# Performance work log

Hardware: AMD Instinct MI355X
Metric: run time of the kernel (lower is better)

Reference implementation:

```python
import jax, jax.numpy as jnp
import numpy as np

EMBED = 1024
HEADS = 16
HEAD_DIM = EMBED // HEADS
HIDDEN = 4096
EPS = 1e-5


def setup_inputs() -> dict:
    key = jax.random.key(0)
    ks = jax.random.split(key, 12)
    s_e = 1.0 / np.sqrt(EMBED)
    s_h = 1.0 / np.sqrt(HIDDEN)
    inp = {
        'x': jax.random.normal(ks[0], (2, 2048, EMBED), jnp.float32),
        'Wq': jax.random.uniform(ks[1], (EMBED, EMBED), jnp.float32, -s_e, s_e),
        'bq': jnp.zeros((EMBED,), jnp.float32),
        'Wk': jax.random.uniform(ks[2], (EMBED, EMBED), jnp.float32, -s_e, s_e),
        'bk': jnp.zeros((EMBED,), jnp.float32),
        'Wv': jax.random.uniform(ks[3], (EMBED, EMBED), jnp.float32, -s_e, s_e),
        'bv': jnp.zeros((EMBED,), jnp.float32),
        'Wo': jax.random.uniform(ks[4], (EMBED, EMBED), jnp.float32, -s_e, s_e),
        'bo': jnp.zeros((EMBED,), jnp.float32),
        'g1': jnp.ones((EMBED,), jnp.float32),
        'b1': jnp.zeros((EMBED,), jnp.float32),
        'W1': jax.random.uniform(ks[5], (EMBED, HIDDEN), jnp.float32, -s_e, s_e),
        'bm1': jnp.zeros((HIDDEN,), jnp.float32),
        'W2': jax.random.uniform(ks[6], (HIDDEN, EMBED), jnp.float32, -s_h, s_h),
        'bm2': jnp.zeros((EMBED,), jnp.float32),
        'g2': jnp.ones((EMBED,), jnp.float32),
        'b2': jnp.zeros((EMBED,), jnp.float32),
    }
    return inp


def _layernorm(x, g, b):
    mu = jnp.mean(x, axis=-1, keepdims=True)
    var = jnp.mean(jnp.square(x - mu), axis=-1, keepdims=True)
    return (x - mu) * jax.lax.rsqrt(var + EPS) * g + b


def _attention(x, Wq, bq, Wk, bk, Wv, bv, Wo, bo):
    b, n, d = x.shape
    def split(h):  # [b,n,d] -> [b,H,n,hd]
        return h.reshape(b, n, HEADS, HEAD_DIM).transpose(0, 2, 1, 3)
    q = split(x @ Wq + bq)
    k = split(x @ Wk + bk)
    v = split(x @ Wv + bv)
    # NOTE: original multiplies by sqrt(head_dim) (bug preserved for faithfulness)
    scores = jnp.einsum('bhqd,bhkd->bhqk', q, k) * jnp.sqrt(jnp.float32(HEAD_DIM))
    causal = jnp.tril(jnp.ones((n, n), bool))
    scores = jnp.where(causal, scores, -jnp.inf)
    attn = jax.nn.softmax(scores, axis=-1)
    out = jnp.einsum('bhqk,bhkd->bhqd', attn, v)
    out = out.transpose(0, 2, 1, 3).reshape(b, n, d)
    return out @ Wo + bo


def reference(x, Wq, bq, Wk, bk, Wv, bv, Wo, bo, g1, b1, W1, bm1, W2, bm2, g2, b2):
    res1 = x
    x = _layernorm(_attention(x, Wq, bq, Wk, bk, Wv, bv, Wo, bo), g1, b1) + res1
    res2 = x
    h = jax.nn.gelu(x @ W1 + bm1, approximate=False) @ W2 + bm2
    return _layernorm(h, g2, b2) + res2
```

## Files before the change

kernel.cpp:

```cpp
#include <hip/hip_runtime.h>
#include <stdint.h>

typedef unsigned short u16;
typedef short short8 __attribute__((ext_vector_type(8)));
typedef float f32x4 __attribute__((ext_vector_type(4)));
typedef u16 u16x4 __attribute__((ext_vector_type(4)));
typedef u16 u16x8 __attribute__((ext_vector_type(8)));

#define MODE_F32  0
#define MODE_GELU 2
#define MODE_VT   4

__device__ __forceinline__ float b2f(u16 v) {
    union { uint32_t u; float f; } x; x.u = ((uint32_t)v) << 16; return x.f;
}
__device__ __forceinline__ u16 f2b(float f) {
    union { float f; uint32_t u; } x; x.f = f;
    uint32_t u = x.u;
    return (u16)((u + 0x7FFFu + ((u >> 16) & 1u)) >> 16);
}

#define ASYNC16(gp, lp)                                                        \
    __builtin_amdgcn_global_load_lds(                                          \
        (const __attribute__((address_space(1))) uint32_t*)(const void*)(gp),  \
        (__attribute__((address_space(3))) uint32_t*)(void*)(lp), 16, 0, 0)

#define MFMA16(a, b, c) __builtin_amdgcn_mfma_f32_16x16x32_bf16((a), (b), (c), 0, 0, 0)

__global__ __launch_bounds__(256) void split_f32(
    const float* __restrict__ in, u16* __restrict__ hi, u16* __restrict__ lo)
{
    const int i = (blockIdx.x * 256 + threadIdx.x) * 4;
    f32x4 v = *(const f32x4*)&in[i];
    u16x4 h, l;
    for (int k = 0; k < 4; k++) {
        h[k] = f2b(v[k]);
        l[k] = f2b(v[k] - b2f(h[k]));
    }
    *(u16x4*)&hi[i] = h;
    *(u16x4*)&lo[i] = l;
}

__global__ __launch_bounds__(256) void transpose_f32_bf16(
    const float* __restrict__ in, u16* __restrict__ out, int rows, int cols)
{
    __shared__ float t[32][33];
    const int r0 = blockIdx.y * 32, c0 = blockIdx.x * 32;
    const int tr = threadIdx.x >> 3, tc = (threadIdx.x & 7) * 4;
    f32x4 v = *(const f32x4*)&in[(size_t)(r0 + tr) * cols + c0 + tc];
    for (int i = 0; i < 4; i++) t[tr][tc + i] = v[i];
    __syncthreads();
    u16x4 ov;
    for (int i = 0; i < 4; i++) ov[i] = f2b(t[tc + i][tr]);
    *(u16x4*)&out[(size_t)(c0 + tr) * rows + r0 + tc] = ov;
}

__global__ __launch_bounds__(256) void transpose_split_f32(
    const float* __restrict__ in, u16* __restrict__ hi, u16* __restrict__ lo,
    int rows, int cols)
{
    __shared__ float t[32][33];
    const int r0 = blockIdx.y * 32, c0 = blockIdx.x * 32;
    const int tr = threadIdx.x >> 3, tc = (threadIdx.x & 7) * 4;
    f32x4 v = *(const f32x4*)&in[(size_t)(r0 + tr) * cols + c0 + tc];
    for (int i = 0; i < 4; i++) t[tr][tc + i] = v[i];
    __syncthreads();
    u16x4 hv, lv;
    for (int i = 0; i < 4; i++) {
        const float f = t[tc + i][tr];
        hv[i] = f2b(f);
        lv[i] = f2b(f - b2f(hv[i]));
    }
    const size_t o = (size_t)(c0 + tr) * rows + r0 + tc;
    *(u16x4*)&hi[o] = hv;
    *(u16x4*)&lo[o] = lv;
}

__global__ __launch_bounds__(256) void gemm_qk_x3(
    const u16* __restrict__ Ahi, const u16* __restrict__ Alo,
    const u16* __restrict__ Bhi, const u16* __restrict__ Blo,
    const float* __restrict__ bq, const float* __restrict__ bk,
    u16* __restrict__ Qhi, u16* __restrict__ Qlo,
    u16* __restrict__ Khi, u16* __restrict__ Klo)
{
    const int K = 1024;
    __shared__ __align__(16) u16 SM[32768];
    u16* lAh = SM;          u16* lAl = SM + 8192;
    u16* lBh = SM + 16384;  u16* lBl = SM + 24576;

    const int tid = threadIdx.x;
    const int w = tid >> 6, lane = tid & 63;
    const int lane15 = lane & 15, q = lane >> 4;
    const int tM = blockIdx.y * 128, tN = blockIdx.x * 128;
    const int m0 = (w >> 1) * 64, n0 = (w & 1) * 64;

    f32x4 acc[4][4];
    for (int i = 0; i < 4; i++)
        for (int j = 0; j < 4; j++)
            acc[i][j] = (f32x4){0.f, 0.f, 0.f, 0.f};

    const int pa0 = 2 * w, pa1 = 2 * w + 1;
    const int srow = lane >> 2, sch = lane & 3;
    const u16* Ah = Ahi + (size_t)tM * K;
    const u16* Al = Alo + (size_t)tM * K;
    const u16* Bh = Bhi + (size_t)tN * K;
    const u16* Bl = Blo + (size_t)tN * K;
    const size_t r0 = (size_t)(pa0 * 16 + srow) * K + sch * 8;
    const size_t r1 = (size_t)(pa1 * 16 + srow) * K + sch * 8;

    ASYNC16(Ah + r0, lAh + pa0 * 512);  ASYNC16(Ah + r1, lAh + pa1 * 512);
    ASYNC16(Al + r0, lAl + pa0 * 512);  ASYNC16(Al + r1, lAl + pa1 * 512);
    ASYNC16(Bh + r0, lBh + pa0 * 512);  ASYNC16(Bh + r1, lBh + pa1 * 512);
    ASYNC16(Bl + r0, lBl + pa0 * 512);  ASYNC16(Bl + r1, lBl + pa1 * 512);

    const int NT = K / 32;
    for (int kt = 0; kt < NT; kt++) {
        __syncthreads();
        const int cb = (kt & 1) * 4096, nb = 4096 - cb;
        if (kt + 1 < NT) {
            const int k0 = (kt + 1) * 32;
            ASYNC16(Ah + r0 + k0, lAh + nb + pa0 * 512);  ASYNC16(Ah + r1 + k0, lAh + nb + pa1 * 512);
            ASYNC16(Al + r0 + k0, lAl + nb + pa0 * 512);  ASYNC16(Al + r1 + k0, lAl + nb + pa1 * 512);
            ASYNC16(Bh + r0 + k0, lBh + nb + pa0 * 512);  ASYNC16(Bh + r1 + k0, lBh + nb + pa1 * 512);
            ASYNC16(Bl + r0 + k0, lBl + nb + pa0 * 512);  ASYNC16(Bl + r1 + k0, lBl + nb + pa1 * 512);
        }
        short8 afh[4], afl[4], bfh[4], bfl[4];
        for (int i = 0; i < 4; i++) {
            const int o = cb + (m0 + i * 16 + lane15) * 32 + q * 8;
            afh[i] = *(const short8*)&lAh[o];
            afl[i] = *(const short8*)&lAl[o];
        }
        for (int j = 0; j < 4; j++) {
            const int o = cb + (n0 + j * 16 + lane15) * 32 + q * 8;
            bfh[j] = *(const short8*)&lBh[o];
            bfl[j] = *(const short8*)&lBl[o];
        }
        for (int i = 0; i < 4; i++)
            for (int j = 0; j < 4; j++) {
                acc[i][j] = MFMA16(afh[i], bfh[j], acc[i][j]);
                acc[i][j] = MFMA16(afh[i], bfl[j], acc[i][j]);
                acc[i][j] = MFMA16(afl[i], bfh[j], acc[i][j]);
            }
    }

    const bool isQ = (tN < 1024);
    u16* dhi = isQ ? Qhi : Khi;
    u16* dlo = isQ ? Qlo : Klo;
    const int cN = isQ ? tN : (tN - 1024);
    u16* sC = SM;
    for (int pass = 0; pass < 2; pass++) {
        __syncthreads();
        for (int i = 0; i < 4; i++) {
            const int rl0 = m0 + i * 16 + q * 4;
            for (int j = 0; j < 4; j++) {
                const int cl = n0 + j * 16 + lane15;
                const float bv = isQ ? bq[cN + cl] : bk[cN + cl];
                for (int r = 0; r < 4; r++) {
                    const float v = acc[i][j][r] + bv;
                    const u16 hv = f2b(v);
                    sC[(rl0 + r) * 136 + cl] = pass == 0 ? hv : f2b(v - b2f(hv));
                }
            }
        }
        __syncthreads();
        u16* dst = pass == 0 ? dhi : dlo;
        for (int t8 = 0; t8 < 8; t8++) {
            const int rl = t8 * 16 + (tid >> 4), cl = (tid & 15) * 8;
            *(u16x8*)&dst[(size_t)(tM + rl) * 1024 + cN + cl] = *(const u16x8*)&sC[rl * 136 + cl];
        }
    }
}

__global__ __launch_bounds__(256) void gemm_bt(
    const u16* __restrict__ A, const u16* __restrict__ Bt, const float* __restrict__ bias,
    int M, int N, int K, int mode,
    float* __restrict__ outF, u16* __restrict__ outB, size_t pstride)
{
    __shared__ __align__(16) u16 SM[17408];
    u16* lA = SM;
    u16* lB = SM + 8192;

    const int tid = threadIdx.x;
    const int w = tid >> 6, lane = tid & 63;
    const int lane15 = lane & 15, q = lane >> 4;
    const int tM = blockIdx.y * 128, tN = blockIdx.x * 128;
    const int m0 = (w >> 1) * 64, n0 = (w & 1) * 64;

    const int kchunk = K / gridDim.z;
    const int koff = blockIdx.z * kchunk;
    outF += (size_t)blockIdx.z * pstride;

    f32x4 acc[4][4];
    for (int i = 0; i < 4; i++)
        for (int j = 0; j < 4; j++)
            acc[i][j] = (f32x4){0.f, 0.f, 0.f, 0.f};

    const int pa0 = 2 * w, pa1 = 2 * w + 1;
    const int srow = lane >> 2, sch = lane & 3;
    const u16* Abase = A + (size_t)tM * K + koff;
    const u16* Bbase = Bt + (size_t)tN * K + koff;
    const size_t r0 = (size_t)(pa0 * 16 + srow) * K + sch * 8;
    const size_t r1 = (size_t)(pa1 * 16 + srow) * K + sch * 8;

    ASYNC16(Abase + r0, lA + pa0 * 512);
    ASYNC16(Abase + r1, lA + pa1 * 512);
    ASYNC16(Bbase + r0, lB + pa0 * 512);
    ASYNC16(Bbase + r1, lB + pa1 * 512);

    const int NT = kchunk / 32;
    for (int kt = 0; kt < NT; kt++) {
        __syncthreads();
        const int cb = (kt & 1) * 4096, nb = 4096 - cb;
        if (kt + 1 < NT) {
            const int k0 = (kt + 1) * 32;
            ASYNC16(Abase + r0 + k0, lA + nb + pa0 * 512);
            ASYNC16(Abase + r1 + k0, lA + nb + pa1 * 512);
            ASYNC16(Bbase + r0 + k0, lB + nb + pa0 * 512);
            ASYNC16(Bbase + r1 + k0, lB + nb + pa1 * 512);
        }
        short8 af[4], bf[4];
        for (int i = 0; i < 4; i++) af[i] = *(const short8*)&lA[cb + (m0 + i * 16 + lane15) * 32 + q * 8];
        for (int j = 0; j < 4; j++) bf[j] = *(const short8*)&lB[cb + (n0 + j * 16 + lane15) * 32 + q * 8];
        for (int i = 0; i < 4; i++)
            for (int j = 0; j < 4; j++)
                acc[i][j] = MFMA16(af[i], bf[j], acc[i][j]);
    }

    if (mode == MODE_F32) {
        for (int i = 0; i < 4; i++) {
            const int rb = tM + m0 + i * 16 + q * 4;
            for (int j = 0; j < 4; j++) {
                const int col = tN + n0 + j * 16 + lane15;
                const float bv = (bias && blockIdx.z == 0) ? bias[col] : 0.f;
                for (int r = 0; r < 4; r++)
                    outF[(size_t)(rb + r) * N + col] = acc[i][j][r] + bv;
            }
        }
        return;
    }

    u16* sC = SM;
    __syncthreads();
    if (mode == MODE_GELU) {
        for (int i = 0; i < 4; i++) {
            const int rl0 = m0 + i * 16 + q * 4;
            for (int j = 0; j < 4; j++) {
                const int cl = n0 + j * 16 + lane15;
                const float bv = bias[tN + cl];
                for (int r = 0; r < 4; r++) {
                    float v = acc[i][j][r] + bv;
                    v = 0.5f * v * (1.f + erff(v * 0.70710678118f));
                    sC[(rl0 + r) * 136 + cl] = f2b(v);
                }
            }
        }
        __syncthreads();
        for (int t8 = 0; t8 < 8; t8++) {
            const int rl = t8 * 16 + (tid >> 4), cl = (tid & 15) * 8;
            *(u16x8*)&outB[(size_t)(tM + rl) * N + tN + cl] = *(const u16x8*)&sC[rl * 136 + cl];
        }
    } else {
        for (int i = 0; i < 4; i++) {
            const int rl0 = m0 + i * 16 + q * 4;
            for (int j = 0; j < 4; j++) {
                const int cl = n0 + j * 16 + lane15;
                const float bv = bias[tN + cl];
                for (int r = 0; r < 4; r++)
                    sC[cl * 136 + rl0 + r] = f2b(acc[i][j][r] + bv);
            }
        }
        __syncthreads();
        const int bb = tM >> 11, nbase = tM & 2047;
        for (int t8 = 0; t8 < 8; t8++) {
            const int cl = t8 * 16 + (tid >> 4), rl = (tid & 15) * 8;
            const int colg = tN + cl;
            u16* dst = &outB[((size_t)(bb * 16 + (colg >> 6)) * 64 + (colg & 63)) * 2048 + nbase + rl];
            *(u16x8*)dst = *(const u16x8*)&sC[cl * 136 + rl];
        }
    }
}

__global__ __launch_bounds__(256) void attn_fwd(
    const u16* __restrict__ Qhig, const u16* __restrict__ Qlog,
    const u16* __restrict__ Khig, const u16* __restrict__ Klog,
    const u16* __restrict__ Vtg, u16* __restrict__ Og)
{
    __shared__ u16 lQh[2][2048], lQl[2][2048];
    __shared__ u16 lKh[2][1024], lKl[2][1024];
    __shared__ u16 lV[2048];
    __shared__ u16 lP[4][640];

    const int tid = threadIdx.x, w = tid >> 6, lane = tid & 63;
    const int lane15 = lane & 15, q = lane >> 4;
    const int bh = blockIdx.x >> 4, pair = blockIdx.x & 15;
    const int b = bh >> 4, h = bh & 15;

    const size_t xoff = (size_t)b * 2048 * 1024 + h * 64;
    const u16* Qh_ = Qhig + xoff;
    const u16* Ql_ = Qlog + xoff;
    const u16* Kh_ = Khig + xoff;
    const u16* Kl_ = Klog + xoff;
    const u16* Vbh = Vtg + (size_t)bh * 64 * 2048;
    u16* Obh = Og + xoff;

    const int srow = lane >> 2, sch = lane & 3;
    const float NEG = -3.0e38f;

    for (int half = 0; half < 2; half++) {
        const int qb = half ? (31 - pair) : pair;
        const int qrow0 = qb * 64;
        const int ntiles = 2 * qb + 2;

        for (int ii = 0; ii < 4; ii++) {
            const int id = w * 4 + ii;
            const int idq = id & 7, ks = idq >> 2, p = idq & 3;
            const size_t so = (size_t)(qrow0 + p * 16 + srow) * 1024 + ks * 32 + sch * 8;
            if (id < 8) ASYNC16(Qh_ + so, &lQh[ks][p * 512]);
            else        ASYNC16(Ql_ + so, &lQl[ks][p * 512]);
        }

        f32x4 o[4];
        for (int j = 0; j < 4; j++) o[j] = (f32x4){0.f, 0.f, 0.f, 0.f};
        float mrow[4], lrow[4];
        for (int r = 0; r < 4; r++) { mrow[r] = NEG; lrow[r] = 0.f; }
        short8 aqh0 = {}, aqh1 = {}, aql0 = {}, aql1 = {};
        bool first = true;

        for (int t = 0; t < ntiles; t++) {
            const int kk0 = t * 32;
            for (int ii = 0; ii < 3; ii++) {
                const int id = w * 3 + ii;
                if (id < 8) {
                    const int sel = id >> 2, idk = id & 3, ks = idk >> 1, hh = idk & 1;
                    const size_t so = (size_t)(kk0 + hh * 16 + srow) * 1024 + ks * 32 + sch * 8;
                    if (sel == 0) ASYNC16(Kh_ + so, &lKh[ks][hh * 512]);
                    else          ASYNC16(Kl_ + so, &lKl[ks][hh * 512]);
                } else {
                    const int p = id - 8;
                    ASYNC16(Vbh + (size_t)(p * 16 + srow) * 2048 + kk0 + sch * 8, &lV[p * 512]);
                }
            }
            __syncthreads();
            if (first) {
                const int o0 = (w * 16 + lane15) * 32 + q * 8;
                aqh0 = *(const short8*)&lQh[0][o0];
                aqh1 = *(const short8*)&lQh[1][o0];
                aql0 = *(const short8*)&lQl[0][o0];
                aql1 = *(const short8*)&lQl[1][o0];
                first = false;
            }
            f32x4 s[2];
            for (int sub = 0; sub < 2; sub++) {
                const int ko = (sub * 16 + lane15) * 32 + q * 8;
                short8 bkh0 = *(const short8*)&lKh[0][ko];
                short8 bkh1 = *(const short8*)&lKh[1][ko];
                short8 bkl0 = *(const short8*)&lKl[0][ko];
                short8 bkl1 = *(const short8*)&lKl[1][ko];
                f32x4 z = (f32x4){0.f, 0.f, 0.f, 0.f};
                z = MFMA16(aqh0, bkh0, z);
                z = MFMA16(aqh1, bkh1, z);
                z = MFMA16(aqh0, bkl0, z);
                z = MFMA16(aqh1, bkl1, z);
                z = MFMA16(aql0, bkh0, z);
                z = MFMA16(aql1, bkh1, z);
                s[sub] = z;
            }
            const int rbase = qrow0 + w * 16 + q * 4;
            for (int sub = 0; sub < 2; sub++)
                for (int r = 0; r < 4; r++) {
                    const int key = kk0 + sub * 16 + lane15;
                    float sv = s[sub][r] * 8.0f;
                    if (key > rbase + r) sv = NEG;
                    s[sub][r] = sv;
                }
            float mx[4];
            for (int r = 0; r < 4; r++) mx[r] = fmaxf(s[0][r], s[1][r]);
            for (int d = 1; d < 16; d <<= 1)
                for (int r = 0; r < 4; r++) mx[r] = fmaxf(mx[r], __shfl_xor(mx[r], d));
            float alpha[4];
            for (int r = 0; r < 4; r++) {
                const float mnew = fmaxf(mrow[r], mx[r]);
                alpha[r] = __expf(mrow[r] - mnew);
                mrow[r] = mnew;
            }
            float rsum[4] = {0.f, 0.f, 0.f, 0.f};
            for (int sub = 0; sub < 2; sub++)
                for (int r = 0; r < 4; r++) {
                    const float p = __expf(s[sub][r] - mrow[r]);
                    rsum[r] += p;
                    lP[w][(q * 4 + r) * 40 + sub * 16 + lane15] = f2b(p);
                }
            for (int d = 1; d < 16; d <<= 1)
                for (int r = 0; r < 4; r++) rsum[r] += __shfl_xor(rsum[r], d);
            for (int r = 0; r < 4; r++) lrow[r] = lrow[r] * alpha[r] + rsum[r];
            for (int j = 0; j < 4; j++)
                for (int r = 0; r < 4; r++) o[j][r] *= alpha[r];
            short8 ap = *(const short8*)&lP[w][lane15 * 40 + q * 8];
            for (int j = 0; j < 4; j++) {
                short8 bv = *(const short8*)&lV[(j * 16 + lane15) * 32 + q * 8];
                o[j] = MFMA16(ap, bv, o[j]);
            }
            __syncthreads();
        }
        float inv[4];
        for (int r = 0; r < 4; r++) inv[r] = 1.0f / lrow[r];
        for (int j = 0; j < 4; j++)
            for (int r = 0; r < 4; r++)
                Obh[(size_t)(qrow0 + w * 16 + q * 4 + r) * 1024 + j * 16 + lane15] =
                    f2b(o[j][r] * inv[r]);
    }
}

__global__ __launch_bounds__(256) void ln_res(
    const float* __restrict__ Xa, const float* __restrict__ Xb,
    const float* __restrict__ resF, const u16* __restrict__ resB,
    const float* __restrict__ g, const float* __restrict__ bb,
    u16* __restrict__ outB, float* __restrict__ outF)
{
    const int w = threadIdx.x >> 6, lane = threadIdx.x & 63;
    const int row = blockIdx.x * 4 + w;
    const size_t rowo = (size_t)row * 1024;
    f32x4 v[4];
    float s = 0.f, ss = 0.f;
    for (int i = 0; i < 4; i++) {
        const int c0 = (i * 64 + lane) * 4;
        v[i] = *(const f32x4*)&Xa[rowo + c0];
        if (Xb) {
            f32x4 v2 = *(const f32x4*)&Xb[rowo + c0];
            for (int k = 0; k < 4; k++) v[i][k] += v2[k];
        }
        for (int k = 0; k < 4; k++) { s += v[i][k]; ss += v[i][k] * v[i][k]; }
    }
    for (int d = 1; d < 64; d <<= 1) { s += __shfl_xor(s, d); ss += __shfl_xor(ss, d); }
    const float mu = s * (1.f / 1024.f);
    const float var = ss * (1.f / 1024.f) - mu * mu;
    const float rstd = rsqrtf(var + 1e-5f);
    for (int i = 0; i < 4; i++) {
        const int c0 = (i * 64 + lane) * 4;
        f32x4 gv = *(const f32x4*)&g[c0];
        f32x4 bv = *(const f32x4*)&bb[c0];
        f32x4 rv;
        if (resF) rv = *(const f32x4*)&resF[rowo + c0];
        else {
            u16x4 rb = *(const u16x4*)&resB[rowo + c0];
            for (int k = 0; k < 4; k++) rv[k] = b2f(rb[k]);
        }
        f32x4 ov;
        for (int k = 0; k < 4; k++)
            ov[k] = (v[i][k] - mu) * rstd * gv[k] + bv[k] + rv[k];
        if (outF) *(f32x4*)&outF[rowo + c0] = ov;
        if (outB) {
            u16x4 ob;
            for (int k = 0; k < 4; k++) ob[k] = f2b(ov[k]);
            *(u16x4*)&outB[rowo + c0] = ob;
        }
    }
}

extern "C" void kernel_launch(void* const* d_in, const int* in_sizes, int n_in,
                              void* d_out, int out_size, void* d_ws, size_t ws_size,
                              hipStream_t stream)
{
    const float* x   = (const float*)d_in[0];
    const float* Wq  = (const float*)d_in[1];  const float* bq  = (const float*)d_in[2];
    const float* Wk  = (const float*)d_in[3];  const float* bk  = (const float*)d_in[4];
    const float* Wv  = (const float*)d_in[5];  const float* bv  = (const float*)d_in[6];
    const float* Wo  = (const float*)d_in[7];  const float* bo  = (const float*)d_in[8];
    const float* g1  = (const float*)d_in[9];  const float* b1  = (const float*)d_in[10];
    const float* W1  = (const float*)d_in[11]; const float* bm1 = (const float*)d_in[12];
    const float* W2  = (const float*)d_in[13]; const float* bm2 = (const float*)d_in[14];
    const float* g2  = (const float*)d_in[15]; const float* b2  = (const float*)d_in[16];

    const size_t MB = (size_t)1 << 20;
    char* ws = (char*)d_ws;
    u16* xhi    = (u16*)(ws + 0 * MB);
    u16* xlo    = (u16*)(ws + 8 * MB);
    u16* WqkThi = (u16*)(ws + 16 * MB);
    u16* WqkTlo = (u16*)(ws + 20 * MB);
    u16* WvT    = (u16*)(ws + 24 * MB);
    u16* WoT    = (u16*)(ws + 26 * MB);
    u16* W1T    = (u16*)(ws + 32 * MB);
    u16* W2T    = (u16*)(ws + 40 * MB);
    u16* Qhi    = (u16*)(ws + 48 * MB);
    u16* Qlo    = (u16*)(ws + 56 * MB);
    u16* Khi    = (u16*)(ws + 64 * MB);
    u16* Klo    = (u16*)(ws + 72 * MB);
    u16* Vtb    = (u16*)(ws + 80 * MB);
    u16* aout   = (u16*)(ws + 16 * MB);
    float* O1   = (float*)(ws + 48 * MB);
    float* O2   = (float*)(ws + 64 * MB);
    u16* x1b    = (u16*)(ws + 80 * MB);
    u16* Hb     = (u16*)(ws + 0 * MB);
    float* H2a  = (float*)(ws + 48 * MB);
    float* H2b  = (float*)(ws + 64 * MB);

    split_f32<<<4096, 256, 0, stream>>>(x, xhi, xlo);
    transpose_split_f32<<<dim3(32, 32), 256, 0, stream>>>(Wq, WqkThi, WqkTlo, 1024, 1024);
    transpose_split_f32<<<dim3(32, 32), 256, 0, stream>>>(Wk, WqkThi + 1024 * 1024,
                                                          WqkTlo + 1024 * 1024, 1024, 1024);
    transpose_f32_bf16<<<dim3(32, 32), 256, 0, stream>>>(Wv, WvT, 1024, 1024);
    transpose_f32_bf16<<<dim3(32, 32), 256, 0, stream>>>(Wo, WoT, 1024, 1024);
    transpose_f32_bf16<<<dim3(128, 32), 256, 0, stream>>>(W1, W1T, 1024, 4096);
    transpose_f32_bf16<<<dim3(32, 128), 256, 0, stream>>>(W2, W2T, 4096, 1024);

    gemm_qk_x3<<<dim3(16, 32), 256, 0, stream>>>(xhi, xlo, WqkThi, WqkTlo, bq, bk,
                                                 Qhi, Qlo, Khi, Klo);
    gemm_bt<<<dim3(8, 32), 256, 0, stream>>>(xhi, WvT, bv, 4096, 1024, 1024,
                                             MODE_VT, nullptr, Vtb, 0);

    attn_fwd<<<dim3(512), 256, 0, stream>>>(Qhi, Qlo, Khi, Klo, Vtb, aout);

    gemm_bt<<<dim3(8, 32, 2), 256, 0, stream>>>(aout, WoT, bo, 4096, 1024, 1024,
                                                MODE_F32, O1, nullptr, (size_t)16 * MB / 4);
    ln_res<<<1024, 256, 0, stream>>>(O1, O2, x, nullptr, g1, b1, x1b, nullptr);

    gemm_bt<<<dim3(32, 32), 256, 0, stream>>>(x1b, W1T, bm1, 4096, 4096, 1024,
                                              MODE_GELU, nullptr, Hb, 0);
    gemm_bt<<<dim3(8, 32, 2), 256, 0, stream>>>(Hb, W2T, bm2, 4096, 1024, 4096,
                                                MODE_F32, H2a, nullptr, (size_t)16 * MB / 4);
    ln_res<<<1024, 256, 0, stream>>>(H2a, H2b, nullptr, x1b, g2, b2, nullptr, (float*)d_out);
}
```

Measured before the change: 510.4 us.

## Double-buffer attention K/V tiles, one query block per CTA, fold scale into Q

Attention now double-buffers K and V tiles in LDS, so the next tile's async loads overlap the current tile's compute and only one barrier is needed per iteration. Each block handles a single query block, scheduled longest-first, instead of a paired short/long half, which doubles the grid to 1024 blocks. The score scale of 8*log2(e) is folded into Q when the QK GEMM writes it, so the softmax uses exp2 and skips the per-element multiply. This costs more LDS per block and may lower occupancy, and scaling Q before the hi/lo split slightly changes rounding.

After: 475.5 us. 1.07x faster.

```diff
diff --git a/kernel.cpp b/kernel.cpp
--- a/kernel.cpp
+++ b/kernel.cpp
@@ -10,6 +10,8 @@
 #define MODE_F32  0
 #define MODE_GELU 2
 #define MODE_VT   4
+
+#define QSCALE 11.5415603271f
 
 __device__ __forceinline__ float b2f(u16 v) {
     union { uint32_t u; float f; } x; x.u = ((uint32_t)v) << 16; return x.f;
@@ -147,6 +149,7 @@
     u16* dhi = isQ ? Qhi : Khi;
     u16* dlo = isQ ? Qlo : Klo;
     const int cN = isQ ? tN : (tN - 1024);
+    const float scl = isQ ? QSCALE : 1.0f;
     u16* sC = SM;
     for (int pass = 0; pass < 2; pass++) {
         __syncthreads();
@@ -156,7 +159,7 @@
                 const int cl = n0 + j * 16 + lane15;
                 const float bv = isQ ? bq[cN + cl] : bk[cN + cl];
                 for (int r = 0; r < 4; r++) {
-                    const float v = acc[i][j][r] + bv;
+                    const float v = (acc[i][j][r] + bv) * scl;
                     const u16 hv = f2b(v);
                     sC[(rl0 + r) * 136 + cl] = pass == 0 ? hv : f2b(v - b2f(hv));
                 }
@@ -286,13 +289,14 @@
     const u16* __restrict__ Vtg, u16* __restrict__ Og)
 {
     __shared__ u16 lQh[2][2048], lQl[2][2048];
-    __shared__ u16 lKh[2][1024], lKl[2][1024];
-    __shared__ u16 lV[2048];
+    __shared__ u16 lKh[2][2][1024], lKl[2][2][1024];
+    __shared__ u16 lV[2][2048];
     __shared__ u16 lP[4][640];
 
     const int tid = threadIdx.x, w = tid >> 6, lane = tid & 63;
     const int lane15 = lane & 15, q = lane >> 4;
-    const int bh = blockIdx.x >> 4, pair = blockIdx.x & 15;
+    const int bh = blockIdx.x & 31;
+    const int qb = 31 - (blockIdx.x >> 5);
     const int b = bh >> 4, h = bh & 15;
 
     const size_t xoff = (size_t)b * 2048 * 1024 + h * 64;
@@ -305,110 +309,120 @@
 
     const int srow = lane >> 2, sch = lane & 3;
     const float NEG = -3.0e38f;
-
-    for (int half = 0; half < 2; half++) {
-        const int qb = half ? (31 - pair) : pair;
-        const int qrow0 = qb * 64;
-        const int ntiles = 2 * qb + 2;
-
-        for (int ii = 0; ii < 4; ii++) {
-            const int id = w * 4 + ii;
-            const int idq = id & 7, ks = idq >> 2, p = idq & 3;
-            const size_t so = (size_t)(qrow0 + p * 16 + srow) * 1024 + ks * 32 + sch * 8;
-            if (id < 8) ASYNC16(Qh_ + so, &lQh[ks][p * 512]);
-            else        ASYNC16(Ql_ + so, &lQl[ks][p * 512]);
-        }
-
-        f32x4 o[4];
-        for (int j = 0; j < 4; j++) o[j] = (f32x4){0.f, 0.f, 0.f, 0.f};
-        float mrow[4], lrow[4];
-        for (int r = 0; r < 4; r++) { mrow[r] = NEG; lrow[r] = 0.f; }
-        short8 aqh0 = {}, aqh1 = {}, aql0 = {}, aql1 = {};
-        bool first = true;
-
-        for (int t = 0; t < ntiles; t++) {
-            const int kk0 = t * 32;
+    const int qrow0 = qb * 64;
+    const int ntiles = 2 * qb + 2;
+
+    for (int ii = 0; ii < 4; ii++) {
+        const int id = w * 4 + ii;
+        const int idq = id & 7, ks = idq >> 2, p = idq & 3;
+        const size_t so = (size_t)(qrow0 + p * 16 + srow) * 1024 + ks * 32 + sch * 8;
+        if (id < 8) ASYNC16(Qh_ + so, &lQh[ks][p * 512]);
+        else        ASYNC16(Ql_ + so, &lQl[ks][p * 512]);
+    }
+    for (int ii = 0; ii < 3; ii++) {
+        const int id = w * 3 + ii;
+        if (id < 8) {
+            const int sel = id >> 2, idk = id & 3, ks = idk >> 1, hh = idk & 1;
+            const size_t so = (size_t)(hh * 16 + srow) * 1024 + ks * 32 + sch * 8;
+            if (sel == 0) ASYNC16(Kh_ + so, &lKh[0][ks][hh * 512]);
+            else          ASYNC16(Kl_ + so, &lKl[0][ks][hh * 512]);
+        } else {
+            const int p = id - 8;
+            ASYNC16(Vbh + (size_t)(p * 16 + srow) * 2048 + sch * 8, &lV[0][p * 512]);
+        }
+    }
+
+    f32x4 o[4];
+    for (int j = 0; j < 4; j++) o[j] = (f32x4){0.f, 0.f, 0.f, 0.f};
+    float mrow[4], lrow[4];
+    for (int r = 0; r < 4; r++) { mrow[r] = NEG; lrow[r] = 0.f; }
+    short8 aqh0 = {}, aqh1 = {}, aql0 = {}, aql1 = {};
+    bool first = true;
+
+    for (int t = 0; t < ntiles; t++) {
+        __syncthreads();
+        const int cur = t & 1, nxt = cur ^ 1;
+        if (t + 1 < ntiles) {
+            const int kk1 = (t + 1) * 32;
             for (int ii = 0; ii < 3; ii++) {
                 const int id = w * 3 + ii;
                 if (id < 8) {
                     const int sel = id >> 2, idk = id & 3, ks = idk >> 1, hh = idk & 1;
-                    const size_t so = (size_t)(kk0 + hh * 16 + srow) * 1024 + ks * 32 + sch * 8;
-                    if (sel == 0) ASYNC16(Kh_ + so, &lKh[ks][hh * 512]);
-                    else          ASYNC16(Kl_ + so, &lKl[ks][hh * 512]);
+                    const size_t so = (size_t)(kk1 + hh * 16 + srow) * 1024 + ks * 32 + sch * 8;
+                    if (sel == 0) ASYNC16(Kh_ + so, &lKh[nxt][ks][hh * 512]);
+                    else          ASYNC16(Kl_ + so, &lKl[nxt][ks][hh * 512]);
                 } else {
                     const int p = id - 8;
-                    ASYNC16(Vbh + (size_t)(p * 16 + srow) * 2048 + kk0 + sch * 8, &lV[p * 512]);
+                    ASYNC16(Vbh + (size_t)(p * 16 + srow) * 2048 + kk1 + sch * 8,
+                            &lV[nxt][p * 512]);
                 }
             }
-            __syncthreads();
-            if (first) {
-                const int o0 = (w * 16 + lane15) * 32 + q * 8;
-                aqh0 = *(const short8*)&lQh[0][o0];
-                aqh1 = *(const short8*)&lQh[1][o0];
-                aql0 = *(const short8*)&lQl[0][o0];
-                aql1 = *(const short8*)&lQl[1][o0];
-                first = false;
-            }
-            f32x4 s[2];
-            for (int sub = 0; sub < 2; sub++) {
-                const int ko = (sub * 16 + lane15) * 32 + q * 8;
-                short8 bkh0 = *(const short8*)&lKh[0][ko];
-                short8 bkh1 = *(const short8*)&lKh[1][ko];
-                short8 bkl0 = *(const short8*)&lKl[0][ko];
-                short8 bkl1 = *(const short8*)&lKl[1][ko];
-                f32x4 z = (f32x4){0.f, 0.f, 0.f, 0.f};
-                z = MFMA16(aqh0, bkh0, z);
-                z = MFMA16(aqh1, bkh1, z);
-                z = MFMA16(aqh0, bkl0, z);
-                z = MFMA16(aqh1, bkl1, z);
-                z = MFMA16(aql0, bkh0, z);
-                z = MFMA16(aql1, bkh1, z);
-                s[sub] = z;
-            }
-            const int rbase = qrow0 + w * 16 + q * 4;
-            for (int sub = 0; sub < 2; sub++)
-                for (int r = 0; r < 4; r++) {
-                    const int key = kk0 + sub * 16 + lane15;
-                    float sv = s[sub][r] * 8.0f;
-                    if (key > rbase + r) sv = NEG;
-                    s[sub][r] = sv;
-                }
-            float mx[4];
-            for (int r = 0; r < 4; r++) mx[r] = fmaxf(s[0][r], s[1][r]);
-            for (int d = 1; d < 16; d <<= 1)
-                for (int r = 0; r < 4; r++) mx[r] = fmaxf(mx[r], __shfl_xor(mx[r], d));
-            float alpha[4];
+        }
+        if (first) {
+            const int o0 = (w * 16 + lane15) * 32 + q * 8;
+            aqh0 = *(const short8*)&lQh[0][o0];
+            aqh1 = *(const short8*)&lQh[1][o0];
+            aql0 = *(const short8*)&lQl[0][o0];
+            aql1 = *(const short8*)&lQl[1][o0];
+            first = false;
+        }
+        const int kk0 = t * 32;
+        f32x4 s[2];
+        for (int sub = 0; sub < 2; sub++) {
+            const int ko = (sub * 16 + lane15) * 32 + q * 8;
+            short8 bkh0 = *(const short8*)&lKh[cur][0][ko];
+            short8 bkh1 = *(const short8*)&lKh[cur][1][ko];
+            short8 bkl0 = *(const short8*)&lKl[cur][0][ko];
+            short8 bkl1 = *(const short8*)&lKl[cur][1][ko];
+            f32x4 z = (f32x4){0.f, 0.f, 0.f, 0.f};
+            z = MFMA16(aqh0, bkh0, z);
+            z = MFMA16(aqh1, bkh1, z);
+            z = MFMA16(aqh0, bkl0, z);
+            z = MFMA16(aqh1, bkl1, z);
+            z = MFMA16(aql0, bkh0, z);
+            z = MFMA16(aql1, bkh1, z);
+            s[sub] = z;
+        }
+        const int rbase = qrow0 + w * 16 + q * 4;
+        for (int sub = 0; sub < 2; sub++)
             for (int r = 0; r < 4; r++) {
-                const float mnew = fmaxf(mrow[r], mx[r]);
-                alpha[r] = __expf(mrow[r] - mnew);
-                mrow[r] = mnew;
-            }
-            float rsum[4] = {0.f, 0.f, 0.f, 0.f};
-            for (int sub = 0; sub < 2; sub++)
-                for (int r = 0; r < 4; r++) {
-                    const float p = __expf(s[sub][r] - mrow[r]);
-                    rsum[r] += p;
-                    lP[w][(q * 4 + r) * 40 + sub * 16 + lane15] = f2b(p);
-                }
-            for (int d = 1; d < 16; d <<= 1)
-                for (int r = 0; r < 4; r++) rsum[r] += __shfl_xor(rsum[r], d);
-            for (int r = 0; r < 4; r++) lrow[r] = lrow[r] * alpha[r] + rsum[r];
-            for (int j = 0; j < 4; j++)
-                for (int r = 0; r < 4; r++) o[j][r] *= alpha[r];
-            short8 ap = *(const short8*)&lP[w][lane15 * 40 + q * 8];
-            for (int j = 0; j < 4; j++) {
-                short8 bv = *(const short8*)&lV[(j * 16 + lane15) * 32 + q * 8];
-                o[j] = MFMA16(ap, bv, o[j]);
-            }
-            __syncthreads();
-        }
-        float inv[4];
-        for (int r = 0; r < 4; r++) inv[r] = 1.0f / lrow[r];
+                const int key = kk0 + sub * 16 + lane15;
+                if (key > rbase + r) s[sub][r] = NEG;
+            }
+        float mx[4];
+        for (int r = 0; r < 4; r++) mx[r] = fmaxf(s[0][r], s[1][r]);
+        for (int d = 1; d < 16; d <<= 1)
+            for (int r = 0; r < 4; r++) mx[r] = fmaxf(mx[r], __shfl_xor(mx[r], d));
+        float alpha[4];
+        for (int r = 0; r < 4; r++) {
+            const float mnew = fmaxf(mrow[r], mx[r]);
+            alpha[r] = __builtin_exp2f(mrow[r] - mnew);
+            mrow[r] = mnew;
+        }
+        float rsum[4] = {0.f, 0.f, 0.f, 0.f};
+        for (int sub = 0; sub < 2; sub++)
+            for (int r = 0; r < 4; r++) {
+                const float p = __builtin_exp2f(s[sub][r] - mrow[r]);
+                rsum[r] += p;
+                lP[w][(q * 4 + r) * 40 + sub * 16 + lane15] = f2b(p);
+            }
+        for (int d = 1; d < 16; d <<= 1)
+            for (int r = 0; r < 4; r++) rsum[r] += __shfl_xor(rsum[r], d);
+        for (int r = 0; r < 4; r++) lrow[r] = lrow[r] * alpha[r] + rsum[r];
         for (int j = 0; j < 4; j++)
-            for (int r = 0; r < 4; r++)
-                Obh[(size_t)(qrow0 + w * 16 + q * 4 + r) * 1024 + j * 16 + lane15] =
-                    f2b(o[j][r] * inv[r]);
-    }
+            for (int r = 0; r < 4; r++) o[j][r] *= alpha[r];
+        short8 ap = *(const short8*)&lP[w][lane15 * 40 + q * 8];
+        for (int j = 0; j < 4; j++) {
+            short8 bv = *(const short8*)&lV[cur][(j * 16 + lane15) * 32 + q * 8];
+            o[j] = MFMA16(ap, bv, o[j]);
+        }
+    }
+    float inv[4];
+    for (int r = 0; r < 4; r++) inv[r] = 1.0f / lrow[r];
+    for (int j = 0; j < 4; j++)
+        for (int r = 0; r < 4; r++)
+            Obh[(size_t)(qrow0 + w * 16 + q * 4 + r) * 1024 + j * 16 + lane15] =
+                f2b(o[j][r] * inv[r]);
 }
 
 __global__ __launch_bounds__(256) void ln_res(
@@ -508,7 +522,7 @@
     gemm_bt<<<dim3(8, 32), 256, 0, stream>>>(xhi, WvT, bv, 4096, 1024, 1024,
                                              MODE_VT, nullptr, Vtb, 0);
 
-    attn_fwd<<<dim3(512), 256, 0, stream>>>(Qhi, Qlo, Khi, Klo, Vtb, aout);
+    attn_fwd<<<dim3(1024), 256, 0, stream>>>(Qhi, Qlo, Khi, Klo, Vtb, aout);
 
     gemm_bt<<<dim3(8, 32, 2), 256, 0, stream>>>(aout, WoT, bo, 4096, 1024, 1024,
                                                 MODE_F32, O1, nullptr, (size_t)16 * MB / 4);
```
